# Kernel tuning notes

Hardware: AMD Instinct MI355X
Metric: run time of the kernel (lower is better)

## Reference

```python
import jax, jax.numpy as jnp
import numpy as np

N, L, H, D, NCLS = 8192, 1024, 512, 256, 2


def setup_inputs() -> dict:
    key = jax.random.key(0)
    ks = jax.random.split(key, 11)
    s = 0.02  # xavier-ish init scale
    return {
        "x": jax.random.normal(ks[0], (N, L), jnp.float32),
        "W_fc": jax.random.normal(ks[1], (L, H), jnp.float32) * s,
        "b_fc": jnp.zeros((H,), jnp.float32),
        "W_a": jax.random.normal(ks[2], (H, D), jnp.float32) * s,
        "b_a": jnp.zeros((D,), jnp.float32),
        "W_b": jax.random.normal(ks[3], (H, D), jnp.float32) * s,
        "b_b": jnp.zeros((D,), jnp.float32),
        "W_c": jax.random.normal(ks[4], (D, 1), jnp.float32) * s,
        "b_c": jnp.zeros((1,), jnp.float32),
        "W_cls": jax.random.normal(ks[5], (H, NCLS), jnp.float32) * s,
        "b_cls": jnp.zeros((NCLS,), jnp.float32),
    }


def reference(x, W_fc, b_fc, W_a, b_a, W_b, b_b, W_c, b_c, W_cls, b_cls):
    n = x.shape[0]
    # fc: Linear + ReLU (dropout p=0, eval)
    h = jax.nn.relu(x @ W_fc + b_fc)                      # [N, 512]
    # gated attention net (Attn_Net_Gated, n_classes=1)
    a = jnp.tanh(h @ W_a + b_a)                           # [N, 256]
    b = jax.nn.sigmoid(h @ W_b + b_b)                     # [N, 256]
    scores = ((a * b) @ W_c + b_c)[:, 0]                  # [N] diagonal scores
    # A_raw: the original's wasteful CxNxN diagonal matrix (C=1)
    idx = jnp.arange(n)
    A_raw = jnp.zeros((1, n, n), x.dtype).at[0, idx, idx].set(scores)
    # bag_forward: softmax over all N*N entries (N^2 - N zeros off-diagonal),
    # then M = (A @ h).sum(dim=1). Closed form, numerically stable:
    m = jnp.maximum(jnp.max(scores), jnp.zeros((), x.dtype))
    e = jnp.exp(scores - m)                               # diag exp terms
    e0 = jnp.exp(-m)                                      # off-diag exp(0 - m)
    Z = jnp.sum(e) + (n * n - n) * e0
    s = e / Z                                             # softmaxed diagonal
    # row_i @ h = s_i*h_i + (1/Z)*sum_{j!=i} h_j ; sum over i:
    M = s @ h + ((n - 1) * e0 / Z) * jnp.sum(h, axis=0)   # [512]
    logits = M @ W_cls + b_cls                            # [2]
    return (logits[None, :], A_raw)
```

## Files before the change

kernel.cpp:

```cpp
#include <hip/hip_runtime.h>
#include <stdint.h>

#define NROWS 8192
#define LDIM  1024
#define HDIM  512

typedef __attribute__((ext_vector_type(8))) short short8;
typedef __attribute__((ext_vector_type(4))) float f32x4;
typedef __attribute__((ext_vector_type(4))) unsigned int u32x4;

typedef __attribute__((address_space(3))) unsigned int lds_uint;
typedef const __attribute__((address_space(1))) unsigned int glob_uint;

#define Z_MEGA_START 0L
#define Z_MEGA_CNT   6815744L
#define ZB_MEGA      3328
#define Z_G1_START   6815744L
#define Z_G1_CNT     5242880L
#define ZB_G1        2560
#define Z_G2_START   12058624L
#define Z_G2_CNT     4194304L
#define ZB_G2        2048
#define Z_RW_START   16252928L
#define Z_RW_CNT     524287L
#define ZB_RW        256

__device__ __forceinline__ void llds16(const void* g, void* l) {
  __builtin_amdgcn_global_load_lds((glob_uint*)g, (lds_uint*)l, 16, 0, 0);
}

__device__ __forceinline__ unsigned short f2bf(float f) {
  union { float f; unsigned int u; } c; c.f = f;
  unsigned int u = c.u;
  unsigned int r = (u + 0x7fffu + ((u >> 16) & 1u)) >> 16;
  return (unsigned short)r;
}

__device__ __forceinline__ float bfbits2f(unsigned int hi16) {
  union { unsigned int u; float f; } c; c.u = hi16;
  return c.f;
}

__device__ __forceinline__ void zero_chunks(u32x4* __restrict__ out16, long c0, long c1, int tid) {
  u32x4 z = {0u, 0u, 0u, 0u};
  for (long i = c0 + tid; i < c1; i += 256) out16[i] = z;
}

__global__ __launch_bounds__(256) void mega_bw_kernel(const float* __restrict__ x,
                                                      const float* __restrict__ Wfc,
                                                      const float* __restrict__ Wa,
                                                      const float* __restrict__ Wb,
                                                      unsigned short* __restrict__ xb,
                                                      unsigned short* __restrict__ WfcT,
                                                      unsigned short* __restrict__ WabT,
                                                      float* __restrict__ out) {
  __shared__ float tile[32][33];
  const int bid = blockIdx.x;
  const int tid = threadIdx.x;
  if (bid < ZB_MEGA) {
    long c0 = Z_MEGA_START + (long)bid * 2048;
    long lim = Z_MEGA_START + Z_MEGA_CNT;
    long c1 = c0 + 2048 < lim ? c0 + 2048 : lim;
    zero_chunks((u32x4*)(out + 4), c0, c1, tid);
    if (bid == 0 && tid == 0) {
      out[2] = 0.f; out[3] = 0.f;
      out[67108864] = 0.f; out[67108865] = 0.f;
    }
    return;
  }
  if (bid < ZB_MEGA + 4096) {
    long i = ((long)(bid - ZB_MEGA) * 256 + tid) * 8;
    float4 v0 = *(const float4*)(x + i);
    float4 v1 = *(const float4*)(x + i + 4);
    union { unsigned short s[8]; uint4 u; } o;
    o.s[0] = f2bf(v0.x); o.s[1] = f2bf(v0.y); o.s[2] = f2bf(v0.z); o.s[3] = f2bf(v0.w);
    o.s[4] = f2bf(v1.x); o.s[5] = f2bf(v1.y); o.s[6] = f2bf(v1.z); o.s[7] = f2bf(v1.w);
    *(uint4*)(xb + i) = o.u;
    return;
  }
  int tt = bid - (ZB_MEGA + 4096);
  const float* src; unsigned short* dst; int srcn, dstk, k0, n0; int mode;
  if (tt < 512) {
    src = Wfc; dst = WfcT; srcn = 512; dstk = 1024; mode = 0;
    k0 = (tt >> 4) * 32; n0 = (tt & 15) * 32;
  } else if (tt < 640) {
    int t2 = tt - 512;
    src = Wa; dst = WabT; srcn = 256; dstk = 512; mode = 1;
    k0 = (t2 >> 3) * 32; n0 = (t2 & 7) * 32;
  } else {
    int t2 = tt - 640;
    src = Wb; dst = WabT; srcn = 256; dstk = 512; mode = 2;
    k0 = (t2 >> 3) * 32; n0 = (t2 & 7) * 32;
  }
  int r = tid >> 3, c4 = (tid & 7) * 4;
  float4 v = *(const float4*)(src + (long)(k0 + r) * srcn + n0 + c4);
  tile[r][c4 + 0] = v.x; tile[r][c4 + 1] = v.y; tile[r][c4 + 2] = v.z; tile[r][c4 + 3] = v.w;
  __syncthreads();
  union { unsigned short s[4]; uint2 u; } o;
#pragma unroll
  for (int j = 0; j < 4; ++j) o.s[j] = f2bf(tile[c4 + j][r]);
  int n = n0 + r;
  long crow;
  if (mode == 0) crow = n;
  else crow = (long)(((n >> 4) << 5) + (n & 15) + (mode == 2 ? 16 : 0));
  *(uint2*)(dst + crow * dstk + k0 + c4) = o.u;
}

__global__ __launch_bounds__(256) void gemm1_kernel(const unsigned short* __restrict__ A,
                                                    const unsigned short* __restrict__ Bt,
                                                    const float* __restrict__ bias,
                                                    unsigned short* __restrict__ out,
                                                    int M, int N, int K,
                                                    float* __restrict__ zout) {
  constexpr int BM = 128, BN = 128, BK = 32;
  __shared__ unsigned short sA[2][BM * BK];
  __shared__ unsigned short sB[2][BN * BK];
  const int tid = threadIdx.x;
  const int nbn = N / BN;
  const int ncomp = (M / BM) * nbn;
  if ((int)blockIdx.x >= ncomp) {
    int zb = (int)blockIdx.x - ncomp;
    long c0 = Z_G1_START + (long)zb * 2048;
    long lim = Z_G1_START + Z_G1_CNT;
    long c1 = c0 + 2048 < lim ? c0 + 2048 : lim;
    zero_chunks((u32x4*)(zout + 4), c0, c1, tid);
    return;
  }
  const int lane = tid & 63;
  const int wv = tid >> 6;
  const int wm = wv >> 1;
  const int wn = wv & 1;
  const int bm = blockIdx.x / nbn, bn = blockIdx.x % nbn;
  const int row0 = bm * BM, col0 = bn * BN;

  f32x4 acc[4][4] = {};
  const int nk = K / BK;

  auto stage = [&](int buf, int kt) {
#pragma unroll
    for (int r = 0; r < 2; ++r) {
      int c = r * 256 + tid;
      int arow = c >> 2, acb = (c & 3) * 8;
      const unsigned short* g = A + (long)(row0 + arow) * K + kt * BK + acb;
      unsigned short* l = (unsigned short*)&sA[buf][(r * 256 + wv * 64) * 8];
      llds16(g, l);
    }
#pragma unroll
    for (int r = 0; r < 2; ++r) {
      int c = r * 256 + tid;
      int brow = c >> 2, bcb = (c & 3) * 8;
      const unsigned short* g = Bt + (long)(col0 + brow) * K + kt * BK + bcb;
      unsigned short* l = (unsigned short*)&sB[buf][(r * 256 + wv * 64) * 8];
      llds16(g, l);
    }
  };

  stage(0, 0);
  __syncthreads();

  for (int kt = 0; kt < nk; ++kt) {
    int cur = kt & 1;
    if (kt + 1 < nk) stage(cur ^ 1, kt + 1);
    const unsigned short* bA = sA[cur];
    const unsigned short* bB = sB[cur];
    short8 af[4], bfr[4];
#pragma unroll
    for (int fm = 0; fm < 4; ++fm)
      af[fm] = *(const short8*)&bA[(wm * 64 + fm * 16 + (lane & 15)) * BK + (lane >> 4) * 8];
#pragma unroll
    for (int fn = 0; fn < 4; ++fn)
      bfr[fn] = *(const short8*)&bB[(wn * 64 + fn * 16 + (lane & 15)) * BK + (lane >> 4) * 8];
#pragma unroll
    for (int fm = 0; fm < 4; ++fm)
#pragma unroll
      for (int fn = 0; fn < 4; ++fn)
        acc[fm][fn] = __builtin_amdgcn_mfma_f32_16x16x32_bf16(af[fm], bfr[fn], acc[fm][fn], 0, 0, 0);
    __syncthreads();
  }

#pragma unroll
  for (int fm = 0; fm < 4; ++fm) {
#pragma unroll
    for (int fn = 0; fn < 4; ++fn) {
#pragma unroll
      for (int i = 0; i < 4; ++i) {
        int row = row0 + wm * 64 + fm * 16 + (lane >> 4) * 4 + i;
        int col = col0 + wn * 64 + fn * 16 + (lane & 15);
        float v = acc[fm][fn][i] + bias[col];
        v = v > 0.f ? v : 0.f;
        out[(long)row * N + col] = f2bf(v);
      }
    }
  }
}

__global__ __launch_bounds__(256) void gemm2_fused(const unsigned short* __restrict__ A,
                                                   const unsigned short* __restrict__ Bt,
                                                   const float* __restrict__ ba_,
                                                   const float* __restrict__ bb_,
                                                   const float* __restrict__ Wc,
                                                   float* __restrict__ spart,
                                                   float* __restrict__ zout) {
  constexpr int BM = 128, BN = 128, BK = 32;
  constexpr int M = NROWS, N = HDIM, K = HDIM;
  __shared__ unsigned short sA[2][BM * BK];
  __shared__ unsigned short sB[2][BN * BK];
  const int tid = threadIdx.x;
  const int nbn = N / BN;
  const int ncomp = (M / BM) * nbn;
  if ((int)blockIdx.x >= ncomp) {
    int zb = (int)blockIdx.x - ncomp;
    long c0 = Z_G2_START + (long)zb * 2048;
    long lim = Z_G2_START + Z_G2_CNT;
    long c1 = c0 + 2048 < lim ? c0 + 2048 : lim;
    zero_chunks((u32x4*)(zout + 4), c0, c1, tid);
    return;
  }
  const int lane = tid & 63;
  const int wv = tid >> 6;
  const int wm = wv >> 1;
  const int wn = wv & 1;
  const int bm = blockIdx.x / nbn, bn = blockIdx.x % nbn;
  const int row0 = bm * BM, col0 = bn * BN;

  f32x4 acc[4][4] = {};
  const int nk = K / BK;

  auto stage = [&](int buf, int kt) {
#pragma unroll
    for (int r = 0; r < 2; ++r) {
      int c = r * 256 + tid;
      int arow = c >> 2, acb = (c & 3) * 8;
      const unsigned short* g = A + (long)(row0 + arow) * K + kt * BK + acb;
      unsigned short* l = (unsigned short*)&sA[buf][(r * 256 + wv * 64) * 8];
      llds16(g, l);
    }
#pragma unroll
    for (int r = 0; r < 2; ++r) {
      int c = r * 256 + tid;
      int brow = c >> 2, bcb = (c & 3) * 8;
      const unsigned short* g = Bt + (long)(col0 + brow) * K + kt * BK + bcb;
      unsigned short* l = (unsigned short*)&sB[buf][(r * 256 + wv * 64) * 8];
      llds16(g, l);
    }
  };

  stage(0, 0);
  __syncthreads();

  for (int kt = 0; kt < nk; ++kt) {
    int cur = kt & 1;
    if (kt + 1 < nk) stage(cur ^ 1, kt + 1);
    const unsigned short* bA = sA[cur];
    const unsigned short* bB = sB[cur];
    short8 af[4], bfr[4];
#pragma unroll
    for (int fm = 0; fm < 4; ++fm)
      af[fm] = *(const short8*)&bA[(wm * 64 + fm * 16 + (lane & 15)) * BK + (lane >> 4) * 8];
#pragma unroll
    for (int fn = 0; fn < 4; ++fn)
      bfr[fn] = *(const short8*)&bB[(wn * 64 + fn * 16 + (lane & 15)) * BK + (lane >> 4) * 8];
#pragma unroll
    for (int fm = 0; fm < 4; ++fm)
#pragma unroll
      for (int fn = 0; fn < 4; ++fn)
        acc[fm][fn] = __builtin_amdgcn_mfma_f32_16x16x32_bf16(af[fm], bfr[fn], acc[fm][fn], 0, 0, 0);
    __syncthreads();
  }

  const int colbase = col0 + wn * 64;
  const int d0 = (colbase >> 5) * 16 + (lane & 15);
  float wc0 = Wc[d0],  wc1 = Wc[d0 + 16];
  float av0 = ba_[d0], av1 = ba_[d0 + 16];
  float bv0 = bb_[d0], bv1 = bb_[d0 + 16];
  float* sp = spart + (long)(bn * 2 + wn) * NROWS;
#pragma unroll
  for (int fm = 0; fm < 4; ++fm) {
#pragma unroll
    for (int i = 0; i < 4; ++i) {
      float a0 = acc[fm][0][i] + av0, b0 = acc[fm][1][i] + bv0;
      float a1 = acc[fm][2][i] + av1, b1 = acc[fm][3][i] + bv1;
      float v = tanhf(a0) * (1.f / (1.f + __expf(-b0))) * wc0
              + tanhf(a1) * (1.f / (1.f + __expf(-b1))) * wc1;
#pragma unroll
      for (int off = 1; off < 16; off <<= 1) v += __shfl_xor(v, off);
      if ((lane & 15) == 0) {
        int row = row0 + wm * 64 + fm * 16 + (lane >> 4) * 4 + i;
        sp[row] = v;
      }
    }
  }
}

__global__ __launch_bounds__(256) void redwsum_kernel(const float* __restrict__ spart,
                                                      const float* __restrict__ bc,
                                                      const unsigned short* __restrict__ h,
                                                      float* __restrict__ part,
                                                      float* __restrict__ out) {
  const int b = blockIdx.x;
  const int t = threadIdx.x;
  if (b >= 64) {
    int zb = b - 64;
    long c0 = Z_RW_START + (long)zb * 2048;
    long lim = Z_RW_START + Z_RW_CNT;
    long c1 = c0 + 2048 < lim ? c0 + 2048 : lim;
    zero_chunks((u32x4*)(out + 4), c0, c1, t);
    return;
  }
  __shared__ float sc[NROWS];
  __shared__ float red[256];
  __shared__ float warr[128];
  const float bcv = bc[0];
  float lmax = -1e30f;
  for (int k = t; k < NROWS; k += 256) {
    float s = bcv;
#pragma unroll
    for (int q = 0; q < 8; ++q) s += spart[q * NROWS + k];
    sc[k] = s;
    lmax = fmaxf(lmax, s);
  }
  red[t] = lmax; __syncthreads();
  for (int s = 128; s; s >>= 1) { if (t < s) red[t] = fmaxf(red[t], red[t + s]); __syncthreads(); }
  float m = fmaxf(red[0], 0.f);
  __syncthreads();
  float lsum = 0.f;
  for (int k = t; k < NROWS; k += 256) lsum += __expf(sc[k] - m);
  red[t] = lsum; __syncthreads();
  for (int s = 128; s; s >>= 1) { if (t < s) red[t] += red[t + s]; __syncthreads(); }
  float e0 = __expf(-m);
  float Z = red[0] + 67100672.0f * e0;
  float c0w = 8191.0f * e0 / Z;
  if (t < 128) warr[t] = __expf(sc[b * 128 + t] - m) / Z + c0w;
  __syncthreads();
  float a0 = 0.f, a1 = 0.f;
  for (int i = 0; i < 128; ++i) {
    float wi = warr[i];
    unsigned int hv = *(const unsigned int*)&h[(long)(b * 128 + i) * 512 + t * 2];
    a0 += wi * bfbits2f(hv << 16);
    a1 += wi * bfbits2f(hv & 0xffff0000u);
  }
  part[b * 512 + t * 2] = a0;
  part[b * 512 + t * 2 + 1] = a1;
}

__global__ __launch_bounds__(512) void final_kernel(const float* __restrict__ part,
                                                    const float* __restrict__ spart,
                                                    const float* __restrict__ bc,
                                                    const float* __restrict__ Wcls,
                                                    const float* __restrict__ bcls,
                                                    float* __restrict__ out) {
  const int t = threadIdx.x;
  if (blockIdx.x > 0) {
    if (t < 256) {
      int row = (blockIdx.x - 1) * 256 + t;
      float s = bc[0];
#pragma unroll
      for (int q = 0; q < 8; ++q) s += spart[q * NROWS + row];
      out[2 + 8193L * row] = s;
    }
    return;
  }
  __shared__ float Msh[512];
  float s = 0.f;
  for (int b = 0; b < 64; ++b) s += part[b * 512 + t];
  Msh[t] = s;
  __syncthreads();
  if (t < 64) {
    float p0 = 0.f, p1 = 0.f;
    for (int j = t; j < 512; j += 64) { p0 += Msh[j] * Wcls[j * 2]; p1 += Msh[j] * Wcls[j * 2 + 1]; }
#pragma unroll
    for (int off = 32; off; off >>= 1) { p0 += __shfl_down(p0, off); p1 += __shfl_down(p1, off); }
    if (t == 0) { out[0] = p0 + bcls[0]; out[1] = p1 + bcls[1]; }
  }
}

extern "C" void kernel_launch(void* const* d_in, const int* in_sizes, int n_in,
                              void* d_out, int out_size, void* d_ws, size_t ws_size,
                              hipStream_t stream) {
  const float* x    = (const float*)d_in[0];
  const float* Wfc  = (const float*)d_in[1];
  const float* bfc  = (const float*)d_in[2];
  const float* Wa   = (const float*)d_in[3];
  const float* ba   = (const float*)d_in[4];
  const float* Wb   = (const float*)d_in[5];
  const float* bb   = (const float*)d_in[6];
  const float* Wc   = (const float*)d_in[7];
  const float* bc   = (const float*)d_in[8];
  const float* Wcls = (const float*)d_in[9];
  const float* bcls = (const float*)d_in[10];
  float* out = (float*)d_out;
  char* ws = (char*)d_ws;

  unsigned short* xb    = (unsigned short*)(ws + 0);
  unsigned short* WfcT  = (unsigned short*)(ws + 16777216);
  unsigned short* WabT  = (unsigned short*)(ws + 17825792);
  unsigned short* hbuf  = (unsigned short*)(ws + 18350080);
  float*          spart = (float*)(ws + 26738688);
  float*          part  = (float*)(ws + 27000832);

  mega_bw_kernel<<<ZB_MEGA + 4096 + 768, 256, 0, stream>>>(x, Wfc, Wa, Wb, xb, WfcT, WabT, out);
  gemm1_kernel<<<(NROWS / 128) * (HDIM / 128) + ZB_G1, 256, 0, stream>>>(
      xb, WfcT, bfc, hbuf, NROWS, HDIM, LDIM, out);
  gemm2_fused<<<(NROWS / 128) * (HDIM / 128) + ZB_G2, 256, 0, stream>>>(
      hbuf, WabT, ba, bb, Wc, spart, out);
  redwsum_kernel<<<64 + ZB_RW, 256, 0, stream>>>(spart, bc, hbuf, part, out);
  final_kernel<<<33, 512, 0, stream>>>(part, spart, bc, Wcls, bcls, out);
}
```

Before: 118.3 us.

## Halve GEMM M-tile to 64 and rebalance zero-fill work across kernels

The two GEMM kernels are merged into one templated kernel with a 64x128 tile instead of 128x128. This doubles the compute blocks from 256 to 512 so more CUs are busy on a 256-CU-class GPU. The gemm2 epilogue now writes 16 score partials instead of 8, and the readers sum over 16. The zero-fill of the large A_raw output is repartitioned, putting more blocks in the prep kernel and fewer in the GEMMs, to balance the memset load against compute. Smaller tiles lower data reuse per block and add partial-sum traffic.

```diff
diff --git a/kernel.cpp b/kernel.cpp
--- a/kernel.cpp
+++ b/kernel.cpp
@@ -12,18 +12,15 @@
 typedef __attribute__((address_space(3))) unsigned int lds_uint;
 typedef const __attribute__((address_space(1))) unsigned int glob_uint;
 
-#define Z_MEGA_START 0L
-#define Z_MEGA_CNT   6815744L
-#define ZB_MEGA      3328
-#define Z_G1_START   6815744L
-#define Z_G1_CNT     5242880L
-#define ZB_G1        2560
-#define Z_G2_START   12058624L
-#define Z_G2_CNT     4194304L
-#define ZB_G2        2048
-#define Z_RW_START   16252928L
-#define Z_RW_CNT     524287L
-#define ZB_RW        256
+#define Z_K1_START 0L
+#define ZB_K1      3968
+#define Z_G1_START 8126464L
+#define ZB_G1      2304
+#define Z_G2_START 12845056L
+#define ZB_G2      1280
+#define Z_RW_START 15466496L
+#define ZB_RW      640
+#define Z_END      16777215L
 
 __device__ __forceinline__ void llds16(const void* g, void* l) {
   __builtin_amdgcn_global_load_lds((glob_uint*)g, (lds_uint*)l, 16, 0, 0);
@@ -41,35 +38,35 @@
   return c.f;
 }
 
-__device__ __forceinline__ void zero_chunks(u32x4* __restrict__ out16, long c0, long c1, int tid) {
+__device__ __forceinline__ void zero_duty(float* __restrict__ out, long zstart, int zblk, int tid) {
+  u32x4* out16 = (u32x4*)(out + 4);
+  long c0 = zstart + (long)zblk * 2048;
+  long c1 = c0 + 2048 < Z_END ? c0 + 2048 : Z_END;
   u32x4 z = {0u, 0u, 0u, 0u};
   for (long i = c0 + tid; i < c1; i += 256) out16[i] = z;
 }
 
-__global__ __launch_bounds__(256) void mega_bw_kernel(const float* __restrict__ x,
-                                                      const float* __restrict__ Wfc,
-                                                      const float* __restrict__ Wa,
-                                                      const float* __restrict__ Wb,
-                                                      unsigned short* __restrict__ xb,
-                                                      unsigned short* __restrict__ WfcT,
-                                                      unsigned short* __restrict__ WabT,
-                                                      float* __restrict__ out) {
+__global__ __launch_bounds__(256) void prep_kernel(const float* __restrict__ x,
+                                                   const float* __restrict__ Wfc,
+                                                   const float* __restrict__ Wa,
+                                                   const float* __restrict__ Wb,
+                                                   unsigned short* __restrict__ xb,
+                                                   unsigned short* __restrict__ WfcT,
+                                                   unsigned short* __restrict__ WabT,
+                                                   float* __restrict__ out) {
   __shared__ float tile[32][33];
   const int bid = blockIdx.x;
   const int tid = threadIdx.x;
-  if (bid < ZB_MEGA) {
-    long c0 = Z_MEGA_START + (long)bid * 2048;
-    long lim = Z_MEGA_START + Z_MEGA_CNT;
-    long c1 = c0 + 2048 < lim ? c0 + 2048 : lim;
-    zero_chunks((u32x4*)(out + 4), c0, c1, tid);
+  if (bid < ZB_K1) {
+    zero_duty(out, Z_K1_START, bid, tid);
     if (bid == 0 && tid == 0) {
       out[2] = 0.f; out[3] = 0.f;
       out[67108864] = 0.f; out[67108865] = 0.f;
     }
     return;
   }
-  if (bid < ZB_MEGA + 4096) {
-    long i = ((long)(bid - ZB_MEGA) * 256 + tid) * 8;
+  if (bid < ZB_K1 + 4096) {
+    long i = ((long)(bid - ZB_K1) * 256 + tid) * 8;
     float4 v0 = *(const float4*)(x + i);
     float4 v1 = *(const float4*)(x + i + 4);
     union { unsigned short s[8]; uint4 u; } o;
@@ -78,8 +75,8 @@
     *(uint4*)(xb + i) = o.u;
     return;
   }
-  int tt = bid - (ZB_MEGA + 4096);
-  const float* src; unsigned short* dst; int srcn, dstk, k0, n0; int mode;
+  int tt = bid - (ZB_K1 + 4096);
+  const float* src; unsigned short* dst; int srcn, dstk, k0, n0, mode;
   if (tt < 512) {
     src = Wfc; dst = WfcT; srcn = 512; dstk = 1024; mode = 0;
     k0 = (tt >> 4) * 32; n0 = (tt & 15) * 32;
@@ -100,58 +97,49 @@
 #pragma unroll
   for (int j = 0; j < 4; ++j) o.s[j] = f2bf(tile[c4 + j][r]);
   int n = n0 + r;
-  long crow;
-  if (mode == 0) crow = n;
-  else crow = (long)(((n >> 4) << 5) + (n & 15) + (mode == 2 ? 16 : 0));
+  long crow = (mode == 0) ? (long)n
+                          : (long)(((n >> 4) << 5) + (n & 15) + (mode == 2 ? 16 : 0));
   *(uint2*)(dst + crow * dstk + k0 + c4) = o.u;
 }
 
-__global__ __launch_bounds__(256) void gemm1_kernel(const unsigned short* __restrict__ A,
-                                                    const unsigned short* __restrict__ Bt,
-                                                    const float* __restrict__ bias,
-                                                    unsigned short* __restrict__ out,
-                                                    int M, int N, int K,
-                                                    float* __restrict__ zout) {
-  constexpr int BM = 128, BN = 128, BK = 32;
+template <int EPI>
+__global__ __launch_bounds__(256) void gemm_bt(const unsigned short* __restrict__ A,
+                                               const unsigned short* __restrict__ Bt,
+                                               const float* __restrict__ q0,
+                                               const float* __restrict__ q1,
+                                               const float* __restrict__ q2,
+                                               void* __restrict__ outp,
+                                               int K,
+                                               float* __restrict__ zout, long zstart) {
+  constexpr int BM = 64, BN = 128, BK = 32;
   __shared__ unsigned short sA[2][BM * BK];
   __shared__ unsigned short sB[2][BN * BK];
   const int tid = threadIdx.x;
-  const int nbn = N / BN;
-  const int ncomp = (M / BM) * nbn;
+  constexpr int nbn = HDIM / BN;
+  const int ncomp = (NROWS / BM) * nbn;
   if ((int)blockIdx.x >= ncomp) {
-    int zb = (int)blockIdx.x - ncomp;
-    long c0 = Z_G1_START + (long)zb * 2048;
-    long lim = Z_G1_START + Z_G1_CNT;
-    long c1 = c0 + 2048 < lim ? c0 + 2048 : lim;
-    zero_chunks((u32x4*)(zout + 4), c0, c1, tid);
+    zero_duty(zout, zstart, (int)blockIdx.x - ncomp, tid);
     return;
   }
   const int lane = tid & 63;
   const int wv = tid >> 6;
   const int wm = wv >> 1;
   const int wn = wv & 1;
-  const int bm = blockIdx.x / nbn, bn = blockIdx.x % nbn;
+  const int bm = blockIdx.x >> 2, bn = blockIdx.x & 3;
   const int row0 = bm * BM, col0 = bn * BN;
-
-  f32x4 acc[4][4] = {};
-  const int nk = K / BK;
+  const int nk = K >> 5;
+  const int ldsA = (wv * 64) * 8;
+  const int arow = tid >> 2, acb = (tid & 3) * 8;
+
+  f32x4 acc[2][4] = {};
 
   auto stage = [&](int buf, int kt) {
+    llds16(A + (long)(row0 + arow) * K + kt * BK + acb, (unsigned short*)&sA[buf][ldsA]);
 #pragma unroll
     for (int r = 0; r < 2; ++r) {
       int c = r * 256 + tid;
-      int arow = c >> 2, acb = (c & 3) * 8;
-      const unsigned short* g = A + (long)(row0 + arow) * K + kt * BK + acb;
-      unsigned short* l = (unsigned short*)&sA[buf][(r * 256 + wv * 64) * 8];
-      llds16(g, l);
-    }
-#pragma unroll
-    for (int r = 0; r < 2; ++r) {
-      int c = r * 256 + tid;
-      int brow = c >> 2, bcb = (c & 3) * 8;
-      const unsigned short* g = Bt + (long)(col0 + brow) * K + kt * BK + bcb;
-      unsigned short* l = (unsigned short*)&sB[buf][(r * 256 + wv * 64) * 8];
-      llds16(g, l);
+      llds16(Bt + (long)(col0 + (c >> 2)) * K + kt * BK + (c & 3) * 8,
+             (unsigned short*)&sB[buf][(r * 256 + wv * 64) * 8]);
     }
   };
 
@@ -163,131 +151,56 @@
     if (kt + 1 < nk) stage(cur ^ 1, kt + 1);
     const unsigned short* bA = sA[cur];
     const unsigned short* bB = sB[cur];
-    short8 af[4], bfr[4];
-#pragma unroll
-    for (int fm = 0; fm < 4; ++fm)
-      af[fm] = *(const short8*)&bA[(wm * 64 + fm * 16 + (lane & 15)) * BK + (lane >> 4) * 8];
+    short8 af[2], bfr[4];
+#pragma unroll
+    for (int fm = 0; fm < 2; ++fm)
+      af[fm] = *(const short8*)&bA[(wm * 32 + fm * 16 + (lane & 15)) * BK + (lane >> 4) * 8];
 #pragma unroll
     for (int fn = 0; fn < 4; ++fn)
       bfr[fn] = *(const short8*)&bB[(wn * 64 + fn * 16 + (lane & 15)) * BK + (lane >> 4) * 8];
 #pragma unroll
-    for (int fm = 0; fm < 4; ++fm)
+    for (int fm = 0; fm < 2; ++fm)
 #pragma unroll
       for (int fn = 0; fn < 4; ++fn)
         acc[fm][fn] = __builtin_amdgcn_mfma_f32_16x16x32_bf16(af[fm], bfr[fn], acc[fm][fn], 0, 0, 0);
     __syncthreads();
   }
 
-#pragma unroll
-  for (int fm = 0; fm < 4; ++fm) {
-#pragma unroll
-    for (int fn = 0; fn < 4; ++fn) {
-#pragma unroll
-      for (int i = 0; i < 4; ++i) {
-        int row = row0 + wm * 64 + fm * 16 + (lane >> 4) * 4 + i;
-        int col = col0 + wn * 64 + fn * 16 + (lane & 15);
-        float v = acc[fm][fn][i] + bias[col];
-        v = v > 0.f ? v : 0.f;
-        out[(long)row * N + col] = f2bf(v);
-      }
-    }
-  }
-}
-
-__global__ __launch_bounds__(256) void gemm2_fused(const unsigned short* __restrict__ A,
-                                                   const unsigned short* __restrict__ Bt,
-                                                   const float* __restrict__ ba_,
-                                                   const float* __restrict__ bb_,
-                                                   const float* __restrict__ Wc,
-                                                   float* __restrict__ spart,
-                                                   float* __restrict__ zout) {
-  constexpr int BM = 128, BN = 128, BK = 32;
-  constexpr int M = NROWS, N = HDIM, K = HDIM;
-  __shared__ unsigned short sA[2][BM * BK];
-  __shared__ unsigned short sB[2][BN * BK];
-  const int tid = threadIdx.x;
-  const int nbn = N / BN;
-  const int ncomp = (M / BM) * nbn;
-  if ((int)blockIdx.x >= ncomp) {
-    int zb = (int)blockIdx.x - ncomp;
-    long c0 = Z_G2_START + (long)zb * 2048;
-    long lim = Z_G2_START + Z_G2_CNT;
-    long c1 = c0 + 2048 < lim ? c0 + 2048 : lim;
-    zero_chunks((u32x4*)(zout + 4), c0, c1, tid);
-    return;
-  }
-  const int lane = tid & 63;
-  const int wv = tid >> 6;
-  const int wm = wv >> 1;
-  const int wn = wv & 1;
-  const int bm = blockIdx.x / nbn, bn = blockIdx.x % nbn;
-  const int row0 = bm * BM, col0 = bn * BN;
-
-  f32x4 acc[4][4] = {};
-  const int nk = K / BK;
-
-  auto stage = [&](int buf, int kt) {
-#pragma unroll
-    for (int r = 0; r < 2; ++r) {
-      int c = r * 256 + tid;
-      int arow = c >> 2, acb = (c & 3) * 8;
-      const unsigned short* g = A + (long)(row0 + arow) * K + kt * BK + acb;
-      unsigned short* l = (unsigned short*)&sA[buf][(r * 256 + wv * 64) * 8];
-      llds16(g, l);
-    }
-#pragma unroll
-    for (int r = 0; r < 2; ++r) {
-      int c = r * 256 + tid;
-      int brow = c >> 2, bcb = (c & 3) * 8;
-      const unsigned short* g = Bt + (long)(col0 + brow) * K + kt * BK + bcb;
-      unsigned short* l = (unsigned short*)&sB[buf][(r * 256 + wv * 64) * 8];
-      llds16(g, l);
-    }
-  };
-
-  stage(0, 0);
-  __syncthreads();
-
-  for (int kt = 0; kt < nk; ++kt) {
-    int cur = kt & 1;
-    if (kt + 1 < nk) stage(cur ^ 1, kt + 1);
-    const unsigned short* bA = sA[cur];
-    const unsigned short* bB = sB[cur];
-    short8 af[4], bfr[4];
-#pragma unroll
-    for (int fm = 0; fm < 4; ++fm)
-      af[fm] = *(const short8*)&bA[(wm * 64 + fm * 16 + (lane & 15)) * BK + (lane >> 4) * 8];
-#pragma unroll
-    for (int fn = 0; fn < 4; ++fn)
-      bfr[fn] = *(const short8*)&bB[(wn * 64 + fn * 16 + (lane & 15)) * BK + (lane >> 4) * 8];
-#pragma unroll
-    for (int fm = 0; fm < 4; ++fm)
+  if (EPI == 0) {
+    const float* bias = q0;
+    unsigned short* oh = (unsigned short*)outp;
+#pragma unroll
+    for (int fm = 0; fm < 2; ++fm)
 #pragma unroll
       for (int fn = 0; fn < 4; ++fn)
-        acc[fm][fn] = __builtin_amdgcn_mfma_f32_16x16x32_bf16(af[fm], bfr[fn], acc[fm][fn], 0, 0, 0);
-    __syncthreads();
-  }
-
-  const int colbase = col0 + wn * 64;
-  const int d0 = (colbase >> 5) * 16 + (lane & 15);
-  float wc0 = Wc[d0],  wc1 = Wc[d0 + 16];
-  float av0 = ba_[d0], av1 = ba_[d0 + 16];
-  float bv0 = bb_[d0], bv1 = bb_[d0 + 16];
-  float* sp = spart + (long)(bn * 2 + wn) * NROWS;
-#pragma unroll
-  for (int fm = 0; fm < 4; ++fm) {
-#pragma unroll
-    for (int i = 0; i < 4; ++i) {
-      float a0 = acc[fm][0][i] + av0, b0 = acc[fm][1][i] + bv0;
-      float a1 = acc[fm][2][i] + av1, b1 = acc[fm][3][i] + bv1;
-      float v = tanhf(a0) * (1.f / (1.f + __expf(-b0))) * wc0
-              + tanhf(a1) * (1.f / (1.f + __expf(-b1))) * wc1;
-#pragma unroll
-      for (int off = 1; off < 16; off <<= 1) v += __shfl_xor(v, off);
-      if ((lane & 15) == 0) {
-        int row = row0 + wm * 64 + fm * 16 + (lane >> 4) * 4 + i;
-        sp[row] = v;
-      }
+#pragma unroll
+        for (int i = 0; i < 4; ++i) {
+          int row = row0 + wm * 32 + fm * 16 + (lane >> 4) * 4 + i;
+          int col = col0 + wn * 64 + fn * 16 + (lane & 15);
+          float v = acc[fm][fn][i] + bias[col];
+          v = v > 0.f ? v : 0.f;
+          oh[(long)row * HDIM + col] = f2bf(v);
+        }
+  } else {
+    const float* ba_ = q0; const float* bb_ = q1; const float* Wc_ = q2;
+#pragma unroll
+    for (int g = 0; g < 2; ++g) {
+      const int colg = col0 + wn * 64 + g * 32;
+      const int d0 = (colg >> 5) * 16 + (lane & 15);
+      float wc = Wc_[d0], av = ba_[d0], bv = bb_[d0];
+      float* sp = (float*)outp + (long)(colg >> 5) * NROWS;
+#pragma unroll
+      for (int fm = 0; fm < 2; ++fm)
+#pragma unroll
+        for (int i = 0; i < 4; ++i) {
+          float aa = acc[fm][g * 2 + 0][i] + av;
+          float bbv = acc[fm][g * 2 + 1][i] + bv;
+          float v = tanhf(aa) * (1.f / (1.f + __expf(-bbv))) * wc;
+#pragma unroll
+          for (int off = 1; off < 16; off <<= 1) v += __shfl_xor(v, off);
+          if ((lane & 15) == 0)
+            sp[row0 + wm * 32 + fm * 16 + (lane >> 4) * 4 + i] = v;
+        }
     }
   }
 }
@@ -300,11 +213,7 @@
   const int b = blockIdx.x;
   const int t = threadIdx.x;
   if (b >= 64) {
-    int zb = b - 64;
-    long c0 = Z_RW_START + (long)zb * 2048;
-    long lim = Z_RW_START + Z_RW_CNT;
-    long c1 = c0 + 2048 < lim ? c0 + 2048 : lim;
-    zero_chunks((u32x4*)(out + 4), c0, c1, t);
+    zero_duty(out, Z_RW_START, b - 64, t);
     return;
   }
   __shared__ float sc[NROWS];
@@ -315,7 +224,7 @@
   for (int k = t; k < NROWS; k += 256) {
     float s = bcv;
 #pragma unroll
-    for (int q = 0; q < 8; ++q) s += spart[q * NROWS + k];
+    for (int q = 0; q < 16; ++q) s += spart[q * NROWS + k];
     sc[k] = s;
     lmax = fmaxf(lmax, s);
   }
@@ -355,7 +264,7 @@
       int row = (blockIdx.x - 1) * 256 + t;
       float s = bc[0];
 #pragma unroll
-      for (int q = 0; q < 8; ++q) s += spart[q * NROWS + row];
+      for (int q = 0; q < 16; ++q) s += spart[q * NROWS + row];
       out[2 + 8193L * row] = s;
     }
     return;
@@ -396,13 +305,11 @@
   unsigned short* WabT  = (unsigned short*)(ws + 17825792);
   unsigned short* hbuf  = (unsigned short*)(ws + 18350080);
   float*          spart = (float*)(ws + 26738688);
-  float*          part  = (float*)(ws + 27000832);
-
-  mega_bw_kernel<<<ZB_MEGA + 4096 + 768, 256, 0, stream>>>(x, Wfc, Wa, Wb, xb, WfcT, WabT, out);
-  gemm1_kernel<<<(NROWS / 128) * (HDIM / 128) + ZB_G1, 256, 0, stream>>>(
-      xb, WfcT, bfc, hbuf, NROWS, HDIM, LDIM, out);
-  gemm2_fused<<<(NROWS / 128) * (HDIM / 128) + ZB_G2, 256, 0, stream>>>(
-      hbuf, WabT, ba, bb, Wc, spart, out);
+  float*          part  = (float*)(ws + 27262976);
+
+  prep_kernel<<<ZB_K1 + 4096 + 768, 256, 0, stream>>>(x, Wfc, Wa, Wb, xb, WfcT, WabT, out);
+  gemm_bt<0><<<512 + ZB_G1, 256, 0, stream>>>(xb, WfcT, bfc, nullptr, nullptr, hbuf, LDIM, out, Z_G1_START);
+  gemm_bt<1><<<512 + ZB_G2, 256, 0, stream>>>(hbuf, WabT, ba, bb, Wc, spart, HDIM, out, Z_G2_START);
   redwsum_kernel<<<64 + ZB_RW, 256, 0, stream>>>(spart, bc, hbuf, part, out);
   final_kernel<<<33, 512, 0, stream>>>(part, spart, bc, Wcls, bcls, out);
 }
```

Measured after the change: 115.3 us. -2.5%, faster.
